# Kernel tuning notes

Measured on AMD Instinct MI355X. Metric: run time of the kernel, lower is better.

Reference implementation:

```python
import jax, jax.numpy as jnp
import numpy as np

L, D = 32768, 1024  # timesteps, independent book-feature columns


def setup_inputs() -> dict:
    key = jax.random.key(0)
    k1, k2 = jax.random.split(key)
    data = jax.random.normal(k1, (L, D), dtype=jnp.float32)
    first_offset = jax.random.normal(k2, (1, D), dtype=jnp.float32)
    alpha = jnp.float32(0.01)  # EWMA smoothing constant in (0, 1)
    return {"data": data, "first_offset": first_offset, "alpha": alpha}


def reference(data, first_offset, alpha):
    # Exact math of ewma_vectorized_safe (vmapped over columns):
    #   y_t = (1 - alpha) * y_{t-1} + alpha * x_t,  y_{-1} = first_offset
    # The original implements this with a chunked power-scaled cumsum trick
    # for precision; a single linear scan computes the identical recurrence.
    decay = 1.0 - alpha

    def step(carry, x_t):  # carry: (D,), x_t: (D,)
        y_t = decay * carry + alpha * x_t
        return y_t, y_t

    last, out = jax.lax.scan(step, first_offset[0], data)  # out: (L, D)
    return out, last[None, :]  # matches (out, out[-1:]) with out_axes=(1, 1)
```

## Files before the change

### kernel.cpp

```cpp
#include <hip/hip_runtime.h>


#define LT  32768
#define DC  1024
#define TCH 64
#define CCH (LT / TCH)
#define TPB 256
#define D4  (DC / 4)

__global__ void ewma_phase1(const float4* __restrict__ data4,
                            float4* __restrict__ zend4,
                            const float* __restrict__ alpha_p) {
    const float alpha = alpha_p[0];
    const float decay = 1.0f - alpha;
    const int tid = threadIdx.x;
    const int c = blockIdx.x;
    const float4* p = data4 + (size_t)c * TCH * D4 + tid;
    float z0 = 0.f, z1 = 0.f, z2 = 0.f, z3 = 0.f;
#pragma unroll 8
    for (int i = 0; i < TCH; ++i) {
        float4 x = p[(size_t)i * D4];
        z0 = fmaf(decay, z0, alpha * x.x);
        z1 = fmaf(decay, z1, alpha * x.y);
        z2 = fmaf(decay, z2, alpha * x.z);
        z3 = fmaf(decay, z3, alpha * x.w);
    }
    zend4[c * D4 + tid] = make_float4(z0, z1, z2, z3);
}

__global__ void ewma_phase2(const float* __restrict__ zend,
                            const float* __restrict__ first,
                            float* __restrict__ carry,
                            const float* __restrict__ alpha_p) {
    const float alpha = alpha_p[0];
    const float decay = 1.0f - alpha;
    float r = 1.0f;
    for (int i = 0; i < TCH; ++i) r *= decay;

    const int lane = threadIdx.x & 63;
    const int wave = (blockIdx.x * blockDim.x + threadIdx.x) >> 6;
    const int d = wave;
    constexpr int CPL = CCH / 64;

    float e[CPL];
#pragma unroll
    for (int j = 0; j < CPL; ++j)
        e[j] = zend[(lane * CPL + j) * DC + d];

    float A = 0.f;
#pragma unroll
    for (int j = 0; j < CPL; ++j) A = fmaf(r, A, e[j]);

    float q = 1.f;
    for (int j = 0; j < CPL; ++j) q *= r;

    float y = A;
    float p = q;
#pragma unroll
    for (int o = 1; o < 64; o <<= 1) {
        float prev = __shfl_up(y, o, 64);
        if (lane >= o) y = fmaf(p, prev, y);
        p = p * p;
    }
    float excl = __shfl_up(y, 1, 64);
    if (lane == 0) excl = 0.f;

    float qpow = 1.f;
    {
        float base = q;
        int e2 = lane;
        while (e2) { if (e2 & 1) qpow *= base; base *= base; e2 >>= 1; }
    }
    float S = fmaf(qpow, first[d], excl);

#pragma unroll
    for (int j = 0; j < CPL; ++j) {
        const int c = lane * CPL + j;
        carry[c * DC + d] = S;
        S = fmaf(r, S, e[j]);
    }
}

__global__ void ewma_phase3(const float4* __restrict__ data4,
                            const float4* __restrict__ carry4,
                            float4* __restrict__ out4,
                            float4* __restrict__ out_last4,
                            const float* __restrict__ alpha_p) {
    const float alpha = alpha_p[0];
    const float decay = 1.0f - alpha;
    const int tid = threadIdx.x;
    const int c = blockIdx.x;
    const float4 cin = carry4[c * D4 + tid];
    const float4* p = data4 + (size_t)c * TCH * D4 + tid;
    float4* o = out4 + (size_t)c * TCH * D4 + tid;
    float z0 = 0.f, z1 = 0.f, z2 = 0.f, z3 = 0.f, pw = 1.f;
#pragma unroll 8
    for (int i = 0; i < TCH; ++i) {
        float4 x = p[(size_t)i * D4];
        z0 = fmaf(decay, z0, alpha * x.x);
        z1 = fmaf(decay, z1, alpha * x.y);
        z2 = fmaf(decay, z2, alpha * x.z);
        z3 = fmaf(decay, z3, alpha * x.w);
        pw *= decay;
        float4 yv;
        yv.x = fmaf(pw, cin.x, z0);
        yv.y = fmaf(pw, cin.y, z1);
        yv.z = fmaf(pw, cin.z, z2);
        yv.w = fmaf(pw, cin.w, z3);
        o[(size_t)i * D4] = yv;
    }
    if (c == CCH - 1) {
        float4 yl;
        yl.x = fmaf(pw, cin.x, z0);
        yl.y = fmaf(pw, cin.y, z1);
        yl.z = fmaf(pw, cin.z, z2);
        yl.w = fmaf(pw, cin.w, z3);
        out_last4[tid] = yl;
    }
}

extern "C" void kernel_launch(void* const* d_in, const int* in_sizes, int n_in,
                              void* d_out, int out_size, void* d_ws, size_t ws_size,
                              hipStream_t stream) {
    const float* data    = (const float*)d_in[0];
    const float* first   = (const float*)d_in[1];
    const float* alpha_p = (const float*)d_in[2];
    float* out = (float*)d_out;

    float* zend  = (float*)d_ws;
    float* carry = zend + (size_t)CCH * DC;

    ewma_phase1<<<CCH, TPB, 0, stream>>>(
        (const float4*)data, (float4*)zend, alpha_p);

    ewma_phase2<<<DC / (TPB / 64), TPB, 0, stream>>>(
        zend, first, carry, alpha_p);

    ewma_phase3<<<CCH, TPB, 0, stream>>>(
        (const float4*)data, (const float4*)carry, (float4*)out,
        (float4*)(out + (size_t)LT * DC), alpha_p);
}
```

Before: 74.00 us.

## Replace three-pass chunked scan with single-pass decoupled look-back scan

Measured after the change: 268.8 us. +263.2%, slower.

```diff
diff --git a/kernel.cpp b/kernel.cpp
--- a/kernel.cpp
+++ b/kernel.cpp
@@ -1,122 +1,129 @@
 #include <hip/hip_runtime.h>
 
 
-#define LT  32768
-#define DC  1024
-#define TCH 64
-#define CCH (LT / TCH)
-#define TPB 256
-#define D4  (DC / 4)
+#define LT   32768
+#define DC   1024
+#define TCH  64
+#define CCH  (LT / TCH)
+#define NG   4
+#define CW   256
+#define NBLK (CCH * NG)
 
-__global__ void ewma_phase1(const float4* __restrict__ data4,
-                            float4* __restrict__ zend4,
-                            const float* __restrict__ alpha_p) {
+__device__ __forceinline__ void st_ws(float* p, float v) {
+    __hip_atomic_store(p, v, __ATOMIC_RELAXED, __HIP_MEMORY_SCOPE_AGENT);
+}
+__device__ __forceinline__ float ld_ws(const float* p) {
+    return __hip_atomic_load(p, __ATOMIC_RELAXED, __HIP_MEMORY_SCOPE_AGENT);
+}
+
+__global__ void ewma_clear(unsigned* __restrict__ w, int n) {
+    int i = blockIdx.x * blockDim.x + threadIdx.x;
+    if (i < n)
+        __hip_atomic_store(&w[i], 0u, __ATOMIC_RELAXED, __HIP_MEMORY_SCOPE_AGENT);
+}
+
+__global__ void ewma_scan(const float* __restrict__ data,
+                          const float* __restrict__ first,
+                          const float* __restrict__ alpha_p,
+                          float* __restrict__ out,
+                          unsigned* __restrict__ ticket,
+                          unsigned* __restrict__ flags,
+                          float* __restrict__ agg,
+                          float* __restrict__ pref) {
+    __shared__ unsigned s_bid;
+    __shared__ int s_n;
+    __shared__ int s_pref;
+    const int tid = threadIdx.x;
+    if (tid == 0) s_bid = atomicAdd(ticket, 1u);
+    __syncthreads();
+    const unsigned vb = s_bid;
+    const int c = (int)(vb >> 2);
+    const int g = (int)(vb & 3u);
+    const int col = g * CW + tid;
+    const int chain = g * CCH;
+
     const float alpha = alpha_p[0];
     const float decay = 1.0f - alpha;
-    const int tid = threadIdx.x;
-    const int c = blockIdx.x;
-    const float4* p = data4 + (size_t)c * TCH * D4 + tid;
-    float z0 = 0.f, z1 = 0.f, z2 = 0.f, z3 = 0.f;
-#pragma unroll 8
+    float rT = decay;
+    rT *= rT; rT *= rT; rT *= rT; rT *= rT; rT *= rT; rT *= rT;
+
+    const float* p = data + (size_t)c * TCH * DC + col;
+    float z[TCH];
+    float zz = 0.f;
+#pragma unroll
     for (int i = 0; i < TCH; ++i) {
-        float4 x = p[(size_t)i * D4];
-        z0 = fmaf(decay, z0, alpha * x.x);
-        z1 = fmaf(decay, z1, alpha * x.y);
-        z2 = fmaf(decay, z2, alpha * x.z);
-        z3 = fmaf(decay, z3, alpha * x.w);
+        zz = fmaf(decay, zz, alpha * p[(size_t)i * DC]);
+        z[i] = zz;
     }
-    zend4[c * D4 + tid] = make_float4(z0, z1, z2, z3);
-}
 
-__global__ void ewma_phase2(const float* __restrict__ zend,
-                            const float* __restrict__ first,
-                            float* __restrict__ carry,
-                            const float* __restrict__ alpha_p) {
-    const float alpha = alpha_p[0];
-    const float decay = 1.0f - alpha;
-    float r = 1.0f;
-    for (int i = 0; i < TCH; ++i) r *= decay;
+    if (c > 0 && c < CCH - 1) {
+        st_ws(&agg[(size_t)(chain + c) * CW + tid], zz);
+        __syncthreads();
+        if (tid == 0)
+            __hip_atomic_store(&flags[chain + c], 1u, __ATOMIC_RELEASE,
+                               __HIP_MEMORY_SCOPE_AGENT);
+    }
 
-    const int lane = threadIdx.x & 63;
-    const int wave = (blockIdx.x * blockDim.x + threadIdx.x) >> 6;
-    const int d = wave;
-    constexpr int CPL = CCH / 64;
+    float carry;
+    if (c == 0) {
+        carry = first[col];
+    } else {
+        carry = 0.f;
+        float rp = 1.f;
+        int j = c - 1;
+        for (;;) {
+            if (tid < 64) {
+                int jj = j - tid;
+                unsigned f = 0u;
+                if (jj >= 0)
+                    f = __hip_atomic_load(&flags[chain + jj], __ATOMIC_ACQUIRE,
+                                          __HIP_MEMORY_SCOPE_AGENT);
+                unsigned long long live = __ballot(f != 0u);
+                unsigned long long prm  = __ballot(f == 2u);
+                if (tid == 0) {
+                    unsigned long long notlive = ~live;
+                    int run    = (notlive == 0ull) ? 64 : (__ffsll((long long)notlive) - 1);
+                    int pfirst = (prm == 0ull) ? 64 : (__ffsll((long long)prm) - 1);
+                    if (pfirst < run) { s_n = pfirst + 1; s_pref = 1; }
+                    else             { s_n = run;        s_pref = 0; }
+                }
+            }
+            __syncthreads();
+            const int n  = s_n;
+            const int hp = s_pref;
+            __syncthreads();
+            if (n == 0) { __builtin_amdgcn_s_sleep(2); continue; }
+            for (int k = 0; k < n; ++k) {
+                const float* src = (hp && k == n - 1) ? pref : agg;
+                float v = ld_ws(&src[(size_t)(chain + j - k) * CW + tid]);
+                carry = fmaf(rp, v, carry);
+                rp *= rT;
+            }
+            j -= n;
+            if (hp) break;
+        }
+    }
 
-    float e[CPL];
+    if (c < CCH - 1) {
+        float y_end = fmaf(rT, carry, zz);
+        st_ws(&pref[(size_t)(chain + c) * CW + tid], y_end);
+        __syncthreads();
+        if (tid == 0)
+            __hip_atomic_store(&flags[chain + c], 2u, __ATOMIC_RELEASE,
+                               __HIP_MEMORY_SCOPE_AGENT);
+    }
+
+    float* o = out + (size_t)c * TCH * DC + col;
+    float w = decay;
+    float y = 0.f;
 #pragma unroll
-    for (int j = 0; j < CPL; ++j)
-        e[j] = zend[(lane * CPL + j) * DC + d];
-
-    float A = 0.f;
-#pragma unroll
-    for (int j = 0; j < CPL; ++j) A = fmaf(r, A, e[j]);
-
-    float q = 1.f;
-    for (int j = 0; j < CPL; ++j) q *= r;
-
-    float y = A;
-    float p = q;
-#pragma unroll
-    for (int o = 1; o < 64; o <<= 1) {
-        float prev = __shfl_up(y, o, 64);
-        if (lane >= o) y = fmaf(p, prev, y);
-        p = p * p;
+    for (int i = 0; i < TCH; ++i) {
+        y = fmaf(w, carry, z[i]);
+        o[(size_t)i * DC] = y;
+        w *= decay;
     }
-    float excl = __shfl_up(y, 1, 64);
-    if (lane == 0) excl = 0.f;
-
-    float qpow = 1.f;
-    {
-        float base = q;
-        int e2 = lane;
-        while (e2) { if (e2 & 1) qpow *= base; base *= base; e2 >>= 1; }
-    }
-    float S = fmaf(qpow, first[d], excl);
-
-#pragma unroll
-    for (int j = 0; j < CPL; ++j) {
-        const int c = lane * CPL + j;
-        carry[c * DC + d] = S;
-        S = fmaf(r, S, e[j]);
-    }
-}
-
-__global__ void ewma_phase3(const float4* __restrict__ data4,
-                            const float4* __restrict__ carry4,
-                            float4* __restrict__ out4,
-                            float4* __restrict__ out_last4,
-                            const float* __restrict__ alpha_p) {
-    const float alpha = alpha_p[0];
-    const float decay = 1.0f - alpha;
-    const int tid = threadIdx.x;
-    const int c = blockIdx.x;
-    const float4 cin = carry4[c * D4 + tid];
-    const float4* p = data4 + (size_t)c * TCH * D4 + tid;
-    float4* o = out4 + (size_t)c * TCH * D4 + tid;
-    float z0 = 0.f, z1 = 0.f, z2 = 0.f, z3 = 0.f, pw = 1.f;
-#pragma unroll 8
-    for (int i = 0; i < TCH; ++i) {
-        float4 x = p[(size_t)i * D4];
-        z0 = fmaf(decay, z0, alpha * x.x);
-        z1 = fmaf(decay, z1, alpha * x.y);
-        z2 = fmaf(decay, z2, alpha * x.z);
-        z3 = fmaf(decay, z3, alpha * x.w);
-        pw *= decay;
-        float4 yv;
-        yv.x = fmaf(pw, cin.x, z0);
-        yv.y = fmaf(pw, cin.y, z1);
-        yv.z = fmaf(pw, cin.z, z2);
-        yv.w = fmaf(pw, cin.w, z3);
-        o[(size_t)i * D4] = yv;
-    }
-    if (c == CCH - 1) {
-        float4 yl;
-        yl.x = fmaf(pw, cin.x, z0);
-        yl.y = fmaf(pw, cin.y, z1);
-        yl.z = fmaf(pw, cin.z, z2);
-        yl.w = fmaf(pw, cin.w, z3);
-        out_last4[tid] = yl;
-    }
+    if (c == CCH - 1)
+        out[(size_t)LT * DC + col] = y;
 }
 
 extern "C" void kernel_launch(void* const* d_in, const int* in_sizes, int n_in,
@@ -127,16 +134,14 @@
     const float* alpha_p = (const float*)d_in[2];
     float* out = (float*)d_out;
 
-    float* zend  = (float*)d_ws;
-    float* carry = zend + (size_t)CCH * DC;
+    float* agg  = (float*)d_ws;
+    float* pref = agg + (size_t)NG * CCH * CW;
+    unsigned* flags  = (unsigned*)(pref + (size_t)NG * CCH * CW);
+    unsigned* ticket = flags + NG * CCH;
 
-    ewma_phase1<<<CCH, TPB, 0, stream>>>(
-        (const float4*)data, (float4*)zend, alpha_p);
+    const int nclear = NG * CCH + 1;
+    ewma_clear<<<(nclear + 255) / 256, 256, 0, stream>>>(flags, nclear);
 
-    ewma_phase2<<<DC / (TPB / 64), TPB, 0, stream>>>(
-        zend, first, carry, alpha_p);
-
-    ewma_phase3<<<CCH, TPB, 0, stream>>>(
-        (const float4*)data, (const float4*)carry, (float4*)out,
-        (float4*)(out + (size_t)LT * DC), alpha_p);
+    ewma_scan<<<NBLK, 256, 0, stream>>>(
+        data, first, alpha_p, out, ticket, flags, agg, pref);
 }
```
